# Kernel optimization log

Measured on AMD Instinct MI355X. Metric: run time of the kernel, lower is better.

The kernel has to match this reference:

```python
import jax, jax.numpy as jnp
import numpy as np

NUM_HEADS = 8
D_MODEL = 128
MAX_LEN = 500  # RelativePositionalEncoding default


def setup_inputs() -> dict:
    key = jax.random.key(0)
    ks = jax.random.split(key, 13)
    B, S, D = 4, 1024, D_MODEL
    d = {
        'query': jax.random.normal(ks[0], (B, S, D), jnp.float32),
        'key': jax.random.normal(ks[1], (B, S, D), jnp.float32),
        'value': jax.random.normal(ks[2], (B, S, D), jnp.float32),
        # nn.Linear weights stored as (out, in), bias (out,)
        'Wq': jax.random.normal(ks[3], (D, D), jnp.float32) * 0.05,
        'bq': jax.random.normal(ks[4], (D,), jnp.float32) * 0.05,
        'Wk': jax.random.normal(ks[5], (D, D), jnp.float32) * 0.05,
        'bk': jax.random.normal(ks[6], (D,), jnp.float32) * 0.05,
        'Wv': jax.random.normal(ks[7], (D, D), jnp.float32) * 0.05,
        'bv': jax.random.normal(ks[8], (D,), jnp.float32) * 0.05,
        'Wo': jax.random.normal(ks[9], (D, D), jnp.float32) * 0.05,
        'bo': jax.random.normal(ks[10], (D,), jnp.float32) * 0.05,
        # embeddings_table: (2*max_len+1, d_model)
        'emb_table': jax.random.normal(ks[11], (2 * MAX_LEN + 1, D), jnp.float32) * 0.05,
    }
    return d


def reference(query, key, value, Wq, bq, Wk, bk, Wv, bv, Wo, bo, emb_table):
    B, S, D = query.shape
    H = NUM_HEADS
    hd = D // H

    def proj(x, W, b):
        # nn.Linear: x @ W.T + b, then split heads -> [B,H,S,hd]
        return (x @ W.T + b).reshape(B, S, H, hd).transpose(0, 2, 1, 3)

    Q = proj(query, Wq, bq)
    K = proj(key, Wk, bk)
    V = proj(value, Wv, bv)

    scores = jnp.einsum('bhqd,bhkd->bhqk', Q, K) / jnp.sqrt(jnp.float32(hd))

    # relative position bias: table gather (S,S,D) -> (S,S,H,hd);
    # batch dim of the torch expand is redundant, so contract directly.
    r = jnp.arange(S)
    rel_idx = jnp.clip(r[None, :] - r[:, None], -MAX_LEN, MAX_LEN) + MAX_LEN  # (S,S)
    E = emb_table[rel_idx].reshape(S, S, H, hd)  # (q,k,h,d)
    scores = scores + jnp.einsum('bhqd,qkhd->bhqk', Q, E)

    attn = jax.nn.softmax(scores + 1e-9, axis=-1)
    out = jnp.einsum('bhqk,bhkd->bhqd', attn, V)
    out = out.transpose(0, 2, 1, 3).reshape(B, S, D)
    return out @ Wo.T + bo
```

## Files before the change

kernel.cpp:

```cpp
#include <hip/hip_runtime.h>

#define NH 8
#define HD 16
#define SLEN 1024
#define BATCH 4
#define MAXL 500
#define NSEG 8
#define KTILES_PER_SEG 4

typedef float f32x4  __attribute__((ext_vector_type(4)));
typedef float f32x16 __attribute__((ext_vector_type(16)));
typedef short s16x8  __attribute__((ext_vector_type(8)));
typedef short s16x4  __attribute__((ext_vector_type(4)));

#if defined(__has_builtin)
#if __has_builtin(__builtin_amdgcn_mfma_f32_32x32x8bf16_1k)
#define HAS_PV_REG 1
#endif
#endif
#ifndef HAS_PV_REG
#define HAS_PV_REG 0
#endif

__device__ inline ushort f2bf(float f) {
    uint u = __builtin_bit_cast(uint, f);
    u = (u + 0x7fffu + ((u >> 16) & 1u)) >> 16;
    return (ushort)u;
}
__device__ inline float bf2f(ushort h) {
    uint u = ((uint)h) << 16;
    return __builtin_bit_cast(float, u);
}

__global__ __launch_bounds__(256) void prep_bf16(
    const float* __restrict__ xq, const float* __restrict__ xk, const float* __restrict__ xv,
    const float* __restrict__ Wq, const float* __restrict__ Wk,
    const float* __restrict__ Wv, const float* __restrict__ Wo,
    const float* __restrict__ emb,
    ushort* __restrict__ xqb, ushort* __restrict__ xkb, ushort* __restrict__ xvb,
    ushort* __restrict__ wqb, ushort* __restrict__ wkb,
    ushort* __restrict__ wvb, ushort* __restrict__ wob,
    ushort* __restrict__ embb)
{
    const int XTOT = 3 * 524288;
    const int WTOT = 4 * 16384;
    const int ETOT = (2 * MAXL + 1) * 128;
    int e0 = (blockIdx.x * 256 + threadIdx.x) * 8;
    const float* src;
    ushort* dst;
    int off;
    if (e0 < XTOT) {
        int which = e0 >> 19; off = e0 & 524287;
        src = which == 0 ? xq : which == 1 ? xk : xv;
        dst = which == 0 ? xqb : which == 1 ? xkb : xvb;
    } else if (e0 < XTOT + WTOT) {
        int t = e0 - XTOT; int which = t >> 14; off = t & 16383;
        src = which == 0 ? Wq : which == 1 ? Wk : which == 2 ? Wv : Wo;
        dst = which == 0 ? wqb : which == 1 ? wkb : which == 2 ? wvb : wob;
    } else if (e0 < XTOT + WTOT + ETOT) {
        off = e0 - XTOT - WTOT; src = emb; dst = embb;
    } else {
        return;
    }
    const float4 a = *(const float4*)&src[off];
    const float4 b = *(const float4*)&src[off + 4];
    ushort tmp[8] = {f2bf(a.x), f2bf(a.y), f2bf(a.z), f2bf(a.w),
                     f2bf(b.x), f2bf(b.y), f2bf(b.z), f2bf(b.w)};
    *(s16x8*)&dst[off] = *(const s16x8*)tmp;
}

__global__ __launch_bounds__(64) void qkv_gemm(
    const ushort* __restrict__ xqb, const ushort* __restrict__ xkb, const ushort* __restrict__ xvb,
    const ushort* __restrict__ wqb, const ushort* __restrict__ wkb, const ushort* __restrict__ wvb,
    const float* __restrict__ bq, const float* __restrict__ bk, const float* __restrict__ bv,
    ushort* __restrict__ Qh, ushort* __restrict__ Kh, ushort* __restrict__ Vt)
{
    const int mode = blockIdx.y;
    const ushort* X = mode == 0 ? xqb : mode == 1 ? xkb : xvb;
    const ushort* W = mode == 0 ? wqb : mode == 1 ? wkb : wvb;
    const float* bb = mode == 0 ? bq : mode == 1 ? bk : bv;

    const int l = threadIdx.x;
    const int row = l & 15, kh = l >> 4;
    const int mt = blockIdx.x >> 2, nq = blockIdx.x & 3;
    const int m0 = mt * 32, n0 = nq * 32;

    s16x8 af[2][4], bfr[2][4];
    #pragma unroll
    for (int ms = 0; ms < 2; ++ms)
        #pragma unroll
        for (int ki = 0; ki < 4; ++ki)
            af[ms][ki] = *(const s16x8*)&X[(size_t)(m0 + 16*ms + row) * 128 + 32*ki + 8*kh];
    #pragma unroll
    for (int ns = 0; ns < 2; ++ns)
        #pragma unroll
        for (int ki = 0; ki < 4; ++ki)
            bfr[ns][ki] = *(const s16x8*)&W[(size_t)(n0 + 16*ns + row) * 128 + 32*ki + 8*kh];

    f32x4 acc[2][2];
    #pragma unroll
    for (int ms = 0; ms < 2; ++ms)
        #pragma unroll
        for (int ns = 0; ns < 2; ++ns)
            #pragma unroll
            for (int r = 0; r < 4; ++r) acc[ms][ns][r] = 0.f;

    #pragma unroll
    for (int ki = 0; ki < 4; ++ki)
        #pragma unroll
        for (int ms = 0; ms < 2; ++ms)
            #pragma unroll
            for (int ns = 0; ns < 2; ++ns)
                acc[ms][ns] = __builtin_amdgcn_mfma_f32_16x16x32_bf16(af[ms][ki], bfr[ns][ki], acc[ms][ns], 0, 0, 0);

    const float scale = (mode == 1) ? 0.25f : 1.0f;
    const int b = m0 >> 10;
    #pragma unroll
    for (int ns = 0; ns < 2; ++ns) {
        const int n = n0 + 16*ns + row;
        const int hh = n >> 4, d = n & 15;
        const float bias = bb[n];
        #pragma unroll
        for (int ms = 0; ms < 2; ++ms) {
            if (mode == 2) {
                ushort4 pk;
                pk.x = f2bf(acc[ms][ns][0] + bias);
                pk.y = f2bf(acc[ms][ns][1] + bias);
                pk.z = f2bf(acc[ms][ns][2] + bias);
                pk.w = f2bf(acc[ms][ns][3] + bias);
                const int s0 = (m0 & 1023) + 16*ms + kh * 4;
                *(ushort4*)&Vt[((size_t)((b*8 + hh)*16 + d)) * SLEN + s0] = pk;
            } else {
                ushort* dst = (mode == 0) ? Qh : Kh;
                #pragma unroll
                for (int r = 0; r < 4; ++r) {
                    const int mm = m0 + 16*ms + kh * 4 + r;
                    const int s = mm & 1023;
                    dst[((size_t)(b*8 + hh) * SLEN + s) * HD + d] = f2bf((acc[ms][ns][r] + bias) * scale);
                }
            }
        }
    }
}

__global__ __launch_bounds__(256) void attn_mfma(
    const ushort* __restrict__ Qh, const ushort* __restrict__ Kh,
    const ushort* __restrict__ Vtg, const ushort* __restrict__ emb_bf,
    float* __restrict__ mp, float* __restrict__ lp, float* __restrict__ op)
{
    __shared__ __align__(16) ushort Rl[4][64][36];
    __shared__ float scb[4][32];
#if !HAS_PV_REG
    __shared__ __align__(16) ushort Pl[4][32][40];
#endif

    const int tid = threadIdx.x;
    const int wid = tid >> 6, lane = tid & 63;
    const int hi = lane >> 5, q = lane & 31;
    const int bh = blockIdx.y, h = bh & 7;
    const int q0b = blockIdx.x * 128;
    const int q0w = q0b + wid * 32;
    const int seg = blockIdx.z;

    const s16x8 qf = *(const s16x8*)&Qh[((size_t)bh * SLEN + q0w + q) * HD + 8 * hi];

    float cq_hi = 0.f, cq_lo = 0.f;
    {
        const s16x8 ehi = *(const s16x8*)&emb_bf[(size_t)(2 * MAXL) * 128 + h * HD + 8 * hi];
        const s16x8 elo = *(const s16x8*)&emb_bf[h * HD + 8 * hi];
        #pragma unroll
        for (int j = 0; j < 8; ++j) {
            cq_hi += bf2f((ushort)qf[j]) * bf2f((ushort)ehi[j]);
            cq_lo += bf2f((ushort)qf[j]) * bf2f((ushort)elo[j]);
        }
        cq_hi += __shfl_xor(cq_hi, 32);
        cq_lo += __shfl_xor(cq_lo, 32);
    }

#if HAS_PV_REG
    f32x16 acc;
    #pragma unroll
    for (int i = 0; i < 16; ++i) acc[i] = 0.f;
#else
    f32x4 o0, o1;
    #pragma unroll
    for (int r = 0; r < 4; ++r) { o0[r] = 0.f; o1[r] = 0.f; }
#endif
    float m = -1e30f, l = 0.f;

    for (int kt = seg * KTILES_PER_SEG; kt < (seg + 1) * KTILES_PER_SEG; ++kt) {
        const int k0 = kt * 32;
        const int relbase = k0 - q0b - 127;
        const bool clampHi = (relbase >= MAXL);
        const bool clampLo = (relbase + 159 <= -MAXL);

        const s16x8 kf = *(const s16x8*)&Kh[((size_t)bh * SLEN + k0 + q) * HD + 8 * hi];
        f32x16 sa;
        #pragma unroll
        for (int i = 0; i < 16; ++i) sa[i] = 0.f;
        sa = __builtin_amdgcn_mfma_f32_32x32x16_bf16(kf, qf, sa, 0, 0, 0);

        float p[16];
        if (!(clampHi || clampLo)) {
            const int j0w = 96 - 32 * wid;
            #pragma unroll
            for (int st = 0; st < 2; ++st) {
                int rel = relbase + j0w + 32 * st + q;
                rel = rel < -MAXL ? -MAXL : (rel > MAXL ? MAXL : rel);
                const s16x8 ef = *(const s16x8*)&emb_bf[(size_t)(rel + MAXL) * 128 + h * HD + 8 * hi];
                f32x16 ra;
                #pragma unroll
                for (int i = 0; i < 16; ++i) ra[i] = 0.f;
                ra = __builtin_amdgcn_mfma_f32_32x32x16_bf16(qf, ef, ra, 0, 0, 0);
                #pragma unroll
                for (int g = 0; g < 4; ++g) {
                    ushort4 pk;
                    pk.x = f2bf(ra[4*g + 0]); pk.y = f2bf(ra[4*g + 1]);
                    pk.z = f2bf(ra[4*g + 2]); pk.w = f2bf(ra[4*g + 3]);
                    *(ushort4*)&Rl[wid][32*st + q][8*g + 4*hi] = pk;
                }
            }
            #pragma unroll
            for (int r = 0; r < 16; ++r) {
                const int krow = (r & 3) + 8 * (r >> 2) + 4 * hi;
                p[r] = sa[r] + bf2f(Rl[wid][krow - q + 31][q]);
            }
        } else {
            const float cq = clampHi ? cq_hi : cq_lo;
            #pragma unroll
            for (int r = 0; r < 16; ++r) p[r] = sa[r] + cq;
        }

        float tm = -1e30f;
        #pragma unroll
        for (int r = 0; r < 16; ++r) tm = fmaxf(tm, p[r]);
        tm = fmaxf(tm, __shfl_xor(tm, 32));
        const float mn = fmaxf(m, tm);
        const float scf = __expf(m - mn);
        float ls = 0.f;
        #pragma unroll
        for (int r = 0; r < 16; ++r) { p[r] = __expf(p[r] - mn); ls += p[r]; }
        ls += __shfl_xor(ls, 32);
        l = l * scf + ls;
        m = mn;
        scb[wid][q] = scf;

#if HAS_PV_REG
        #pragma unroll
        for (int r = 0; r < 16; ++r) acc[r] *= scb[wid][(r & 3) + 8 * (r >> 2) + 4 * hi];
        const int d = lane & 15;
        __builtin_amdgcn_s_setprio(1);
        #pragma unroll
        for (int s = 0; s < 4; ++s) {
            ushort pk4[4] = {f2bf(p[4*s + 0]), f2bf(p[4*s + 1]),
                             f2bf(p[4*s + 2]), f2bf(p[4*s + 3])};
            const s16x4 ap = *(const s16x4*)pk4;
            const s16x4 vb = *(const s16x4*)&Vtg[((size_t)(bh * 16 + d)) * SLEN + k0 + 8*s + 4*hi];
            acc = __builtin_amdgcn_mfma_f32_32x32x8bf16_1k(ap, vb, acc, 0, 0, 0);
        }
        __builtin_amdgcn_s_setprio(0);
#else
        #pragma unroll
        for (int g = 0; g < 4; ++g) {
            ushort4 pk;
            pk.x = f2bf(p[4*g + 0]); pk.y = f2bf(p[4*g + 1]);
            pk.z = f2bf(p[4*g + 2]); pk.w = f2bf(p[4*g + 3]);
            *(ushort4*)&Pl[wid][q][8*g + 4*hi] = pk;
        }
        const s16x8 vf = *(const s16x8*)&Vtg[((size_t)(bh * 16 + (lane & 15))) * SLEN + k0 + 8 * (lane >> 4)];
        {
            const s16x8 pa = *(const s16x8*)&Pl[wid][lane & 15][8 * (lane >> 4)];
            #pragma unroll
            for (int r = 0; r < 4; ++r) o0[r] *= scb[wid][(lane >> 4) * 4 + r];
            o0 = __builtin_amdgcn_mfma_f32_16x16x32_bf16(pa, vf, o0, 0, 0, 0);
        }
        {
            const s16x8 pa = *(const s16x8*)&Pl[wid][16 + (lane & 15)][8 * (lane >> 4)];
            #pragma unroll
            for (int r = 0; r < 4; ++r) o1[r] *= scb[wid][16 + (lane >> 4) * 4 + r];
            o1 = __builtin_amdgcn_mfma_f32_16x16x32_bf16(pa, vf, o1, 0, 0, 0);
        }
#endif
    }

    const size_t pbase = (size_t)(seg * 32 + bh) * SLEN;
    if (hi == 0) {
        mp[pbase + q0w + q] = m;
        lp[pbase + q0w + q] = l;
    }
#if HAS_PV_REG
    if ((lane & 31) < 16) {
        const int d = lane & 31;
        #pragma unroll
        for (int r = 0; r < 16; ++r) {
            const int qp = (r & 3) + 8 * (r >> 2) + 4 * hi;
            op[(pbase + q0w + qp) * HD + d] = acc[r];
        }
    }
#else
    #pragma unroll
    for (int half = 0; half < 2; ++half) {
        #pragma unroll
        for (int r = 0; r < 4; ++r) {
            const int qp = half * 16 + (lane >> 4) * 4 + r;
            op[(pbase + q0w + qp) * HD + (lane & 15)] = (half ? o1[r] : o0[r]);
        }
    }
#endif
}

__global__ __launch_bounds__(256) void merge_kernel(
    const float* __restrict__ mp, const float* __restrict__ lp,
    const float* __restrict__ op, ushort* __restrict__ ohbf)
{
    const int idx = blockIdx.x * 256 + threadIdx.x;
    const int d = idx & 15;
    const int row = idx >> 4;
    const int bh = row >> 10, q = row & 1023;
    const int h = bh & 7, b = bh >> 3;

    float ms[NSEG];
    float M = -1e30f;
    #pragma unroll
    for (int s = 0; s < NSEG; ++s) {
        ms[s] = mp[(size_t)s * 32 * SLEN + row];
        M = fmaxf(M, ms[s]);
    }
    float L = 0.f, acc = 0.f;
    #pragma unroll
    for (int s = 0; s < NSEG; ++s) {
        const float w = __expf(ms[s] - M);
        L += lp[(size_t)s * 32 * SLEN + row] * w;
        acc += op[((size_t)s * 32 * SLEN + row) * HD + d] * w;
    }
    ohbf[((size_t)(b * SLEN + q)) * 128 + h * HD + d] = f2bf(acc / L);
}

__global__ __launch_bounds__(64) void out_gemm(
    const ushort* __restrict__ ohbf, const ushort* __restrict__ wob,
    const float* __restrict__ bo, float* __restrict__ out)
{
    const int l = threadIdx.x;
    const int row = l & 15, kh = l >> 4;
    const int mt = blockIdx.x >> 2, nq = blockIdx.x & 3;
    const int m0 = mt * 32, n0 = nq * 32;

    s16x8 af[2][4], bfr[2][4];
    #pragma unroll
    for (int ms = 0; ms < 2; ++ms)
        #pragma unroll
        for (int ki = 0; ki < 4; ++ki)
            af[ms][ki] = *(const s16x8*)&ohbf[(size_t)(m0 + 16*ms + row) * 128 + 32*ki + 8*kh];
    #pragma unroll
    for (int ns = 0; ns < 2; ++ns)
        #pragma unroll
        for (int ki = 0; ki < 4; ++ki)
            bfr[ns][ki] = *(const s16x8*)&wob[(size_t)(n0 + 16*ns + row) * 128 + 32*ki + 8*kh];

    f32x4 acc[2][2];
    #pragma unroll
    for (int ms = 0; ms < 2; ++ms)
        #pragma unroll
        for (int ns = 0; ns < 2; ++ns)
            #pragma unroll
            for (int r = 0; r < 4; ++r) acc[ms][ns][r] = 0.f;

    #pragma unroll
    for (int ki = 0; ki < 4; ++ki)
        #pragma unroll
        for (int ms = 0; ms < 2; ++ms)
            #pragma unroll
            for (int ns = 0; ns < 2; ++ns)
                acc[ms][ns] = __builtin_amdgcn_mfma_f32_16x16x32_bf16(af[ms][ki], bfr[ns][ki], acc[ms][ns], 0, 0, 0);

    #pragma unroll
    for (int ns = 0; ns < 2; ++ns) {
        const int n = n0 + 16*ns + row;
        const float bias = bo[n];
        #pragma unroll
        for (int ms = 0; ms < 2; ++ms)
            #pragma unroll
            for (int r = 0; r < 4; ++r) {
                const int mm = m0 + 16*ms + kh * 4 + r;
                out[(size_t)mm * 128 + n] = acc[ms][ns][r] + bias;
            }
    }
}

extern "C" void kernel_launch(void* const* d_in, const int* in_sizes, int n_in,
                              void* d_out, int out_size, void* d_ws, size_t ws_size,
                              hipStream_t stream)
{
    const float* query  = (const float*)d_in[0];
    const float* key_in = (const float*)d_in[1];
    const float* value  = (const float*)d_in[2];
    const float* Wq = (const float*)d_in[3];
    const float* bq = (const float*)d_in[4];
    const float* Wk = (const float*)d_in[5];
    const float* bk = (const float*)d_in[6];
    const float* Wv = (const float*)d_in[7];
    const float* bv = (const float*)d_in[8];
    const float* Wo = (const float*)d_in[9];
    const float* bo = (const float*)d_in[10];
    const float* emb = (const float*)d_in[11];
    float* out = (float*)d_out;

    const size_t TEN = (size_t)BATCH * NH * SLEN * HD;
    const size_t WE  = 16384;
    const size_t EE  = (size_t)(2 * MAXL + 1) * 128;
    const size_t ROWS = (size_t)32 * SLEN;

    ushort* qh   = (ushort*)d_ws;
    ushort* kh   = qh + TEN;
    ushort* vtg  = kh + TEN;
    ushort* xqb  = vtg + TEN;
    ushort* xkb  = xqb + TEN;
    ushort* xvb  = xkb + TEN;
    ushort* wqb  = xvb + TEN;
    ushort* wkb  = wqb + WE;
    ushort* wvb  = wkb + WE;
    ushort* wob  = wvb + WE;
    ushort* embb = wob + WE;
    ushort* ohbf = embb + EE;
    float*  mp   = (float*)(ohbf + TEN);
    float*  lp   = mp + NSEG * ROWS;
    float*  op   = lp + NSEG * ROWS;

    prep_bf16<<<863, 256, 0, stream>>>(query, key_in, value, Wq, Wk, Wv, Wo, emb,
                                       xqb, xkb, xvb, wqb, wkb, wvb, wob, embb);
    qkv_gemm<<<dim3(512, 3), 64, 0, stream>>>(xqb, xkb, xvb, wqb, wkb, wvb,
                                              bq, bk, bv, qh, kh, vtg);
    attn_mfma<<<dim3(8, 32, NSEG), 256, 0, stream>>>(qh, kh, vtg, embb, mp, lp, op);
    merge_kernel<<<(32 * SLEN * HD) / 256, 256, 0, stream>>>(mp, lp, op, ohbf);
    out_gemm<<<512, 64, 0, stream>>>(ohbf, wob, bo, out);
}
```

Baseline: 126.3 us.

## Fuse bf16 conversion into QKV GEMM and merge into output projection

Removes the separate prep_bf16 pass: the QKV GEMM now loads fp32 inputs and weights and converts them to bf16 in registers, and an extra grid slice converts the embedding table. The split-softmax merge is fused with the output GEMM, staging the merged head outputs in shared memory instead of a global bf16 buffer. This cuts two kernel launches and the global round-trips of the converted tensors. In exchange, weights are reconverted redundantly by every block, and merge_out runs only 128 blocks, which may underuse the GPU.

```diff
diff --git a/kernel.cpp b/kernel.cpp
--- a/kernel.cpp
+++ b/kernel.cpp
@@ -31,56 +31,36 @@
     uint u = ((uint)h) << 16;
     return __builtin_bit_cast(float, u);
 }
-
-__global__ __launch_bounds__(256) void prep_bf16(
+__device__ inline s16x8 ld8bf(const float* __restrict__ src) {
+    const float4 a = *(const float4*)src;
+    const float4 b = *(const float4*)(src + 4);
+    ushort tmp[8] = {f2bf(a.x), f2bf(a.y), f2bf(a.z), f2bf(a.w),
+                     f2bf(b.x), f2bf(b.y), f2bf(b.z), f2bf(b.w)};
+    return *(const s16x8*)tmp;
+}
+
+__global__ __launch_bounds__(64) void qkv_gemm(
     const float* __restrict__ xq, const float* __restrict__ xk, const float* __restrict__ xv,
-    const float* __restrict__ Wq, const float* __restrict__ Wk,
-    const float* __restrict__ Wv, const float* __restrict__ Wo,
+    const float* __restrict__ Wq, const float* __restrict__ Wk, const float* __restrict__ Wv,
+    const float* __restrict__ bq, const float* __restrict__ bk, const float* __restrict__ bv,
     const float* __restrict__ emb,
-    ushort* __restrict__ xqb, ushort* __restrict__ xkb, ushort* __restrict__ xvb,
-    ushort* __restrict__ wqb, ushort* __restrict__ wkb,
-    ushort* __restrict__ wvb, ushort* __restrict__ wob,
+    ushort* __restrict__ Qh, ushort* __restrict__ Kh, ushort* __restrict__ Vt,
     ushort* __restrict__ embb)
 {
-    const int XTOT = 3 * 524288;
-    const int WTOT = 4 * 16384;
-    const int ETOT = (2 * MAXL + 1) * 128;
-    int e0 = (blockIdx.x * 256 + threadIdx.x) * 8;
-    const float* src;
-    ushort* dst;
-    int off;
-    if (e0 < XTOT) {
-        int which = e0 >> 19; off = e0 & 524287;
-        src = which == 0 ? xq : which == 1 ? xk : xv;
-        dst = which == 0 ? xqb : which == 1 ? xkb : xvb;
-    } else if (e0 < XTOT + WTOT) {
-        int t = e0 - XTOT; int which = t >> 14; off = t & 16383;
-        src = which == 0 ? Wq : which == 1 ? Wk : which == 2 ? Wv : Wo;
-        dst = which == 0 ? wqb : which == 1 ? wkb : which == 2 ? wvb : wob;
-    } else if (e0 < XTOT + WTOT + ETOT) {
-        off = e0 - XTOT - WTOT; src = emb; dst = embb;
-    } else {
+    const int mode = blockIdx.y;
+    const int l = threadIdx.x;
+
+    if (mode == 3) {
+        int e0 = (blockIdx.x * 64 + l) * 8;
+        if (e0 < (2 * MAXL + 1) * 128)
+            *(s16x8*)&embb[e0] = ld8bf(&emb[e0]);
         return;
     }
-    const float4 a = *(const float4*)&src[off];
-    const float4 b = *(const float4*)&src[off + 4];
-    ushort tmp[8] = {f2bf(a.x), f2bf(a.y), f2bf(a.z), f2bf(a.w),
-                     f2bf(b.x), f2bf(b.y), f2bf(b.z), f2bf(b.w)};
-    *(s16x8*)&dst[off] = *(const s16x8*)tmp;
-}
-
-__global__ __launch_bounds__(64) void qkv_gemm(
-    const ushort* __restrict__ xqb, const ushort* __restrict__ xkb, const ushort* __restrict__ xvb,
-    const ushort* __restrict__ wqb, const ushort* __restrict__ wkb, const ushort* __restrict__ wvb,
-    const float* __restrict__ bq, const float* __restrict__ bk, const float* __restrict__ bv,
-    ushort* __restrict__ Qh, ushort* __restrict__ Kh, ushort* __restrict__ Vt)
-{
-    const int mode = blockIdx.y;
-    const ushort* X = mode == 0 ? xqb : mode == 1 ? xkb : xvb;
-    const ushort* W = mode == 0 ? wqb : mode == 1 ? wkb : wvb;
+
+    const float* X  = mode == 0 ? xq : mode == 1 ? xk : xv;
+    const float* W  = mode == 0 ? Wq : mode == 1 ? Wk : Wv;
     const float* bb = mode == 0 ? bq : mode == 1 ? bk : bv;
 
-    const int l = threadIdx.x;
     const int row = l & 15, kh = l >> 4;
     const int mt = blockIdx.x >> 2, nq = blockIdx.x & 3;
     const int m0 = mt * 32, n0 = nq * 32;
@@ -90,12 +70,12 @@
     for (int ms = 0; ms < 2; ++ms)
         #pragma unroll
         for (int ki = 0; ki < 4; ++ki)
-            af[ms][ki] = *(const s16x8*)&X[(size_t)(m0 + 16*ms + row) * 128 + 32*ki + 8*kh];
+            af[ms][ki] = ld8bf(&X[(size_t)(m0 + 16*ms + row) * 128 + 32*ki + 8*kh]);
     #pragma unroll
     for (int ns = 0; ns < 2; ++ns)
         #pragma unroll
         for (int ki = 0; ki < 4; ++ki)
-            bfr[ns][ki] = *(const s16x8*)&W[(size_t)(n0 + 16*ns + row) * 128 + 32*ki + 8*kh];
+            bfr[ns][ki] = ld8bf(&W[(size_t)(n0 + 16*ns + row) * 128 + 32*ki + 8*kh]);
 
     f32x4 acc[2][2];
     #pragma unroll
@@ -309,53 +289,73 @@
 #endif
 }
 
-__global__ __launch_bounds__(256) void merge_kernel(
+__global__ __launch_bounds__(256) void merge_out(
     const float* __restrict__ mp, const float* __restrict__ lp,
-    const float* __restrict__ op, ushort* __restrict__ ohbf)
-{
-    const int idx = blockIdx.x * 256 + threadIdx.x;
-    const int d = idx & 15;
-    const int row = idx >> 4;
-    const int bh = row >> 10, q = row & 1023;
-    const int h = bh & 7, b = bh >> 3;
-
-    float ms[NSEG];
-    float M = -1e30f;
-    #pragma unroll
-    for (int s = 0; s < NSEG; ++s) {
-        ms[s] = mp[(size_t)s * 32 * SLEN + row];
-        M = fmaxf(M, ms[s]);
-    }
-    float L = 0.f, acc = 0.f;
-    #pragma unroll
-    for (int s = 0; s < NSEG; ++s) {
-        const float w = __expf(ms[s] - M);
-        L += lp[(size_t)s * 32 * SLEN + row] * w;
-        acc += op[((size_t)s * 32 * SLEN + row) * HD + d] * w;
-    }
-    ohbf[((size_t)(b * SLEN + q)) * 128 + h * HD + d] = f2bf(acc / L);
-}
-
-__global__ __launch_bounds__(64) void out_gemm(
-    const ushort* __restrict__ ohbf, const ushort* __restrict__ wob,
+    const float* __restrict__ op, const float* __restrict__ Wo,
     const float* __restrict__ bo, float* __restrict__ out)
 {
-    const int l = threadIdx.x;
-    const int row = l & 15, kh = l >> 4;
-    const int mt = blockIdx.x >> 2, nq = blockIdx.x & 3;
-    const int m0 = mt * 32, n0 = nq * 32;
+    __shared__ __align__(16) ushort ohs[32][136];
+
+    const int t = threadIdx.x;
+    const int m0 = blockIdx.x * 32;
+    const int b = m0 >> 10;
+
+    {
+        const int r = t >> 3, hh = t & 7;
+        const int s = (m0 + r) & 1023;
+        const int row = (b * 8 + hh) * SLEN + s;
+        float msv[NSEG], w[NSEG];
+        float M = -1e30f;
+        #pragma unroll
+        for (int sg = 0; sg < NSEG; ++sg) {
+            msv[sg] = mp[(size_t)sg * 32 * SLEN + row];
+            M = fmaxf(M, msv[sg]);
+        }
+        float L = 0.f;
+        #pragma unroll
+        for (int sg = 0; sg < NSEG; ++sg) {
+            w[sg] = __expf(msv[sg] - M);
+            L += lp[(size_t)sg * 32 * SLEN + row] * w[sg];
+        }
+        const float inv = 1.f / L;
+        float a[HD];
+        #pragma unroll
+        for (int d = 0; d < HD; ++d) a[d] = 0.f;
+        #pragma unroll
+        for (int sg = 0; sg < NSEG; ++sg) {
+            const float4* src = (const float4*)&op[((size_t)sg * 32 * SLEN + row) * HD];
+            #pragma unroll
+            for (int c = 0; c < 4; ++c) {
+                const float4 v = src[c];
+                a[4*c+0] += v.x * w[sg]; a[4*c+1] += v.y * w[sg];
+                a[4*c+2] += v.z * w[sg]; a[4*c+3] += v.w * w[sg];
+            }
+        }
+        #pragma unroll
+        for (int c = 0; c < 4; ++c) {
+            ushort4 pk;
+            pk.x = f2bf(a[4*c+0] * inv); pk.y = f2bf(a[4*c+1] * inv);
+            pk.z = f2bf(a[4*c+2] * inv); pk.w = f2bf(a[4*c+3] * inv);
+            *(ushort4*)&ohs[r][hh * 16 + 4*c] = pk;
+        }
+    }
+    __syncthreads();
+
+    const int wid = t >> 6, lane = t & 63;
+    const int row = lane & 15, kh = lane >> 4;
+    const int n0 = wid * 32;
 
     s16x8 af[2][4], bfr[2][4];
     #pragma unroll
     for (int ms = 0; ms < 2; ++ms)
         #pragma unroll
         for (int ki = 0; ki < 4; ++ki)
-            af[ms][ki] = *(const s16x8*)&ohbf[(size_t)(m0 + 16*ms + row) * 128 + 32*ki + 8*kh];
+            af[ms][ki] = *(const s16x8*)&ohs[16*ms + row][32*ki + 8*kh];
     #pragma unroll
     for (int ns = 0; ns < 2; ++ns)
         #pragma unroll
         for (int ki = 0; ki < 4; ++ki)
-            bfr[ns][ki] = *(const s16x8*)&wob[(size_t)(n0 + 16*ns + row) * 128 + 32*ki + 8*kh];
+            bfr[ns][ki] = ld8bf(&Wo[(size_t)(n0 + 16*ns + row) * 128 + 32*ki + 8*kh]);
 
     f32x4 acc[2][2];
     #pragma unroll
@@ -406,31 +406,19 @@
     float* out = (float*)d_out;
 
     const size_t TEN = (size_t)BATCH * NH * SLEN * HD;
-    const size_t WE  = 16384;
     const size_t EE  = (size_t)(2 * MAXL + 1) * 128;
     const size_t ROWS = (size_t)32 * SLEN;
 
     ushort* qh   = (ushort*)d_ws;
     ushort* kh   = qh + TEN;
     ushort* vtg  = kh + TEN;
-    ushort* xqb  = vtg + TEN;
-    ushort* xkb  = xqb + TEN;
-    ushort* xvb  = xkb + TEN;
-    ushort* wqb  = xvb + TEN;
-    ushort* wkb  = wqb + WE;
-    ushort* wvb  = wkb + WE;
-    ushort* wob  = wvb + WE;
-    ushort* embb = wob + WE;
-    ushort* ohbf = embb + EE;
-    float*  mp   = (float*)(ohbf + TEN);
+    ushort* embb = vtg + TEN;
+    float*  mp   = (float*)(embb + EE + (EE & 1));
     float*  lp   = mp + NSEG * ROWS;
     float*  op   = lp + NSEG * ROWS;
 
-    prep_bf16<<<863, 256, 0, stream>>>(query, key_in, value, Wq, Wk, Wv, Wo, emb,
-                                       xqb, xkb, xvb, wqb, wkb, wvb, wob, embb);
-    qkv_gemm<<<dim3(512, 3), 64, 0, stream>>>(xqb, xkb, xvb, wqb, wkb, wvb,
-                                              bq, bk, bv, qh, kh, vtg);
+    qkv_gemm<<<dim3(512, 4), 64, 0, stream>>>(
+        query, key_in, value, Wq, Wk, Wv, bq, bk, bv, emb, qh, kh, vtg, embb);
     attn_mfma<<<dim3(8, 32, NSEG), 256, 0, stream>>>(qh, kh, vtg, embb, mp, lp, op);
-    merge_kernel<<<(32 * SLEN * HD) / 256, 256, 0, stream>>>(mp, lp, op, ohbf);
-    out_gemm<<<512, 64, 0, stream>>>(ohbf, wob, bo, out);
-}
+    merge_out<<<128, 256, 0, stream>>>(mp, lp, op, Wo, bo, out);
+}
```

Result: slower. 130.5 us (+3.3%).
